# Kernel tuning notes

Measured on AMD Instinct MI355X. Metric: run time of the kernel, lower is better.

Reference implementation:

```python
import jax, jax.numpy as jnp
import numpy as np

B, T_IN, T_OUT, V, C = 2048, 10, 25, 22, 3
D = V * C            # embed / gru hidden = 66
H = 3                # attention heads
HD = D // H          # head dim = 22
EPS = 1e-5
DIMS = [(C, 64), (64, 32), (32, 64), (64, C)]


def _bn(x, g, b):
    # eval-mode BatchNorm2d with default running stats (mean=0, var=1)
    return x * (g / jnp.sqrt(1.0 + EPS))[None, :, None, None] + b[None, :, None, None]


def _gcn_layer(x, A, Tm, cw, cb, g, bt, rw, rb, rg, rbt, pre):
    # x: (N, Cin, T, V); STSGCN ST_GCNN_layer with 1x1 conv (kernel [1,1])
    res = _bn(jnp.einsum('nctv,oc->notv', x, rw) + rb[None, :, None, None], rg, rbt)
    y = jnp.einsum('nctv,vtq->ncqv', x, Tm)   # temporal mixing
    y = jnp.einsum('nctv,tvw->nctw', y, A)    # spatial (joint) mixing
    y = _bn(jnp.einsum('nctv,oc->notv', y, cw) + cb[None, :, None, None], g, bt)
    y = y + res
    return jnp.where(y >= 0, y, pre * y)      # PReLU (scalar slope)


def setup_inputs() -> dict:
    key = jax.random.key(0)
    ks = iter(jax.random.split(key, 64))
    def rn(shape, s=0.05):
        return jax.random.normal(next(ks), shape, dtype=jnp.float32) * s
    d = {"x": rn((B, T_IN, V, C), 1.0)}
    d["A"] = rn((4, T_IN, V, V), 0.2)
    d["Tm"] = rn((4, V, T_IN, T_IN), 0.3)
    d["pre"] = jnp.full((4,), 0.25, jnp.float32)
    for i, (ci, co) in enumerate(DIMS):
        d[f"cw{i}"] = rn((co, ci), 0.1)
        d[f"cb{i}"] = rn((co,), 0.1)
        d[f"g{i}"] = jnp.ones((co,), jnp.float32)
        d[f"bt{i}"] = jnp.zeros((co,), jnp.float32)
        d[f"rw{i}"] = rn((co, ci), 0.1)
        d[f"rb{i}"] = rn((co,), 0.1)
        d[f"rg{i}"] = jnp.ones((co,), jnp.float32)
        d[f"rbt{i}"] = jnp.zeros((co,), jnp.float32)
    d["gru_wi"] = rn((3 * D, D)); d["gru_wh"] = rn((3 * D, D))
    d["gru_bi"] = rn((3 * D,));   d["gru_bh"] = rn((3 * D,))
    d["qkv_w"] = rn((3 * D, D)); d["qkv_b"] = rn((3 * D,))
    d["ow"] = rn((D, D)); d["ob"] = rn((D,))
    d["lw"] = rn((D, 2 * D)); d["lb"] = rn((D,))
    return d


def _forward(x, A, Tm, pre, cws, cbs, gs, bts, rws, rbs, rgs, rbts,
             gru_wi, gru_wh, gru_bi, gru_bh, qkv_w, qkv_b, ow, ob, lw, lb):
    raw = x.reshape(B, T_IN, D)                 # (N,T,V*C), joint-major flatten
    h = jnp.transpose(x, (0, 3, 1, 2))          # (N,C,T,V)
    for i in range(4):
        h = _gcn_layer(h, A[i], Tm[i], cws[i], cbs[i], gs[i], bts[i],
                       rws[i], rbs[i], rgs[i], rbts[i], pre[i])
    enc = jnp.transpose(h, (0, 2, 3, 1)).reshape(B, T_IN, D)  # (N,T,V*C)

    wq, wk, wv = qkv_w[:D], qkv_w[D:2 * D], qkv_w[2 * D:]
    bq, bk, bv = qkv_b[:D], qkv_b[D:2 * D], qkv_b[2 * D:]
    # K,V of encoder sequence are constant across decode steps: project once
    k = (enc @ wk.T + bk).reshape(B, T_IN, H, HD)
    v = (enc @ wv.T + bv).reshape(B, T_IN, H, HD)
    scale = 1.0 / jnp.sqrt(jnp.float32(HD))

    def gru(inp, hprev):
        gi = inp @ gru_wi.T + gru_bi
        gh = hprev @ gru_wh.T + gru_bh
        ir, iz, inn = jnp.split(gi, 3, axis=-1)
        hr, hz, hn = jnp.split(gh, 3, axis=-1)
        r = jax.nn.sigmoid(ir + hr)
        z = jax.nn.sigmoid(iz + hz)
        n = jnp.tanh(inn + r * hn)
        return (1.0 - z) * n + z * hprev

    def step(carry, _):
        hs, tp = carry
        hs = gru(tp, hs)
        q = ((hs @ wq.T + bq) * scale).reshape(B, H, HD)
        scores = jnp.einsum('bhd,bthd->bht', q, k)
        attn = jax.nn.softmax(scores, axis=-1)
        ctx = jnp.einsum('bht,bthd->bhd', attn, v).reshape(B, D) @ ow.T + ob
        pred = jnp.concatenate([hs, ctx], axis=-1) @ lw.T + lb + tp  # residual
        return (hs, pred), pred

    h0 = enc[:, -1, :]
    tp0 = raw[:, -1, :]
    _, preds = jax.lax.scan(step, (h0, tp0), None, length=T_OUT)
    out = jnp.transpose(preds, (1, 0, 2))       # (N, T_out, D)
    return out.reshape(B, T_OUT, V, C)


def reference(x, A, Tm, pre,
              cw0, cb0, g0, bt0, rw0, rb0, rg0, rbt0,
              cw1, cb1, g1, bt1, rw1, rb1, rg1, rbt1,
              cw2, cb2, g2, bt2, rw2, rb2, rg2, rbt2,
              cw3, cb3, g3, bt3, rw3, rb3, rg3, rbt3,
              gru_wi, gru_wh, gru_bi, gru_bh, qkv_w, qkv_b, ow, ob, lw, lb):
    return _forward(x, A, Tm, pre,
                    [cw0, cw1, cw2, cw3], [cb0, cb1, cb2, cb3],
                    [g0, g1, g2, g3], [bt0, bt1, bt2, bt3],
                    [rw0, rw1, rw2, rw3], [rb0, rb1, rb2, rb3],
                    [rg0, rg1, rg2, rg3], [rbt0, rbt1, rbt2, rbt3],
                    gru_wi, gru_wh, gru_bi, gru_bh, qkv_w, qkv_b, ow, ob, lw, lb)
```

## Files before the change

kernel.cpp:

```cpp
#include <hip/hip_runtime.h>

#define DEV static __device__ __forceinline__


struct EncW {
  const float* cw[4]; const float* cb[4]; const float* g[4]; const float* bt[4];
  const float* rw[4]; const float* rb[4]; const float* rg[4]; const float* rbt[4];
};

template<int CI, int CO, int OGRAN>
DEV void gcn_layer32(int tid,
    const float* __restrict__ cw, const float* __restrict__ cb,
    const float* __restrict__ gg, const float* __restrict__ bt,
    const float* __restrict__ rw, const float* __restrict__ rb,
    const float* __restrict__ rg, const float* __restrict__ rbt,
    const float* __restrict__ TmL, const float* __restrict__ AL, float preL,
    float* __restrict__ act, float* __restrict__ S,
    float* __restrict__ rmul, float* __restrict__ radd,
    float* __restrict__ cmul, float* __restrict__ cadd)
{
  constexpr int COP8 = (CO + 7) & ~7;
  constexpr int NT = (CO / OGRAN) * 55;
  const float inv = 0.99999499987f;

  for (int idx = tid; idx < CI * COP8; idx += 512) {
    int c = idx / COP8, o = idx % COP8;
    S[idx] = (o < CO) ? rw[o * CI + c] : 0.f;
  }
  for (int idx = tid; idx < 64; idx += 512) {
    bool ok = idx < CO;
    float rm = ok ? rg[idx] * inv : 0.f;
    float cm = ok ? gg[idx] * inv : 0.f;
    rmul[idx] = rm;
    radd[idx] = ok ? rb[idx] * rm + rbt[idx] : 0.f;
    cmul[idx] = cm;
    cadd[idx] = ok ? cb[idx] * cm + bt[idx] : 0.f;
  }
  __syncthreads();

  float racc[OGRAN * 4];
  int og = tid / 55, pp = tid % 55;
  if (tid < NT) {
    #pragma unroll
    for (int k = 0; k < OGRAN * 4; ++k) racc[k] = 0.f;
    #pragma unroll 4
    for (int c = 0; c < CI; ++c) {
      const float* wr = S + c * COP8 + og * OGRAN;
      float4 av = *(const float4*)(act + c * 220 + pp * 4);
      float wv[OGRAN];
      if constexpr (OGRAN == 8) {
        float4 w0 = *(const float4*)(wr);
        float4 w1 = *(const float4*)(wr + 4);
        wv[0]=w0.x; wv[1]=w0.y; wv[2]=w0.z; wv[3]=w0.w;
        wv[4]=w1.x; wv[5]=w1.y; wv[6]=w1.z; wv[7]=w1.w;
      } else if constexpr (OGRAN == 4) {
        float4 w0 = *(const float4*)(wr);
        wv[0]=w0.x; wv[1]=w0.y; wv[2]=w0.z; wv[3]=w0.w;
      } else {
        wv[0] = wr[0];
      }
      #pragma unroll
      for (int o = 0; o < OGRAN; ++o) {
        racc[o*4+0] += wv[o]*av.x; racc[o*4+1] += wv[o]*av.y;
        racc[o*4+2] += wv[o]*av.z; racc[o*4+3] += wv[o]*av.w;
      }
    }
    #pragma unroll
    for (int o = 0; o < OGRAN; ++o) {
      float m = rmul[og * OGRAN + o], a = radd[og * OGRAN + o];
      #pragma unroll
      for (int k = 0; k < 4; ++k) racc[o*4+k] = racc[o*4+k]*m + a;
    }
  }
  __syncthreads();

  for (int idx = tid; idx < 2200; idx += 512) {
    int tq = idx / 22, v = idx % 22;
    int t = tq / 10, q = tq % 10;
    S[idx] = TmL[v * 100 + t * 10 + q];
  }
  __syncthreads();

  for (int idx = tid; idx < CI * 11; idx += 512) {
    int v2 = idx % 11, c = idx / 11;
    float* base = act + c * 220 + v2 * 2;
    float xin[10][2];
    #pragma unroll
    for (int t = 0; t < 10; ++t) { xin[t][0] = base[t*22]; xin[t][1] = base[t*22+1]; }
    float ya[10][2];
    #pragma unroll
    for (int q = 0; q < 10; ++q) { ya[q][0] = 0.f; ya[q][1] = 0.f; }
    #pragma unroll
    for (int t = 0; t < 10; ++t) {
      const float* tm = S + t * 220 + v2 * 2;
      #pragma unroll
      for (int q = 0; q < 10; ++q) {
        ya[q][0] += tm[q*22]   * xin[t][0];
        ya[q][1] += tm[q*22+1] * xin[t][1];
      }
    }
    #pragma unroll
    for (int q = 0; q < 10; ++q) { base[q*22] = ya[q][0]; base[q*22+1] = ya[q][1]; }
  }
  __syncthreads();

  for (int idx = tid; idx < 4840; idx += 512) S[idx] = AL[idx];
  __syncthreads();

  for (int idx = tid; idx < CI * 10; idx += 512) {
    int t = idx % 10, c = idx / 10;
    float* row = act + c * 220 + t * 22;
    float yin[22];
    #pragma unroll
    for (int v = 0; v < 22; ++v) yin[v] = row[v];
    float za[22];
    #pragma unroll
    for (int w = 0; w < 22; ++w) za[w] = 0.f;
    #pragma unroll 2
    for (int v = 0; v < 22; ++v) {
      const float* ar = S + (t * 22 + v) * 22;
      float y0 = yin[v];
      #pragma unroll
      for (int w = 0; w < 22; ++w) za[w] += y0 * ar[w];
    }
    #pragma unroll
    for (int w = 0; w < 22; ++w) row[w] = za[w];
  }
  __syncthreads();

  for (int idx = tid; idx < CI * COP8; idx += 512) {
    int c = idx / COP8, o = idx % COP8;
    S[idx] = (o < CO) ? cw[o * CI + c] : 0.f;
  }
  __syncthreads();

  float cacc[OGRAN * 4];
  if (tid < NT) {
    #pragma unroll
    for (int k = 0; k < OGRAN * 4; ++k) cacc[k] = 0.f;
    #pragma unroll 4
    for (int c = 0; c < CI; ++c) {
      const float* wr = S + c * COP8 + og * OGRAN;
      float4 av = *(const float4*)(act + c * 220 + pp * 4);
      float wv[OGRAN];
      if constexpr (OGRAN == 8) {
        float4 w0 = *(const float4*)(wr);
        float4 w1 = *(const float4*)(wr + 4);
        wv[0]=w0.x; wv[1]=w0.y; wv[2]=w0.z; wv[3]=w0.w;
        wv[4]=w1.x; wv[5]=w1.y; wv[6]=w1.z; wv[7]=w1.w;
      } else if constexpr (OGRAN == 4) {
        float4 w0 = *(const float4*)(wr);
        wv[0]=w0.x; wv[1]=w0.y; wv[2]=w0.z; wv[3]=w0.w;
      } else {
        wv[0] = wr[0];
      }
      #pragma unroll
      for (int o = 0; o < OGRAN; ++o) {
        cacc[o*4+0] += wv[o]*av.x; cacc[o*4+1] += wv[o]*av.y;
        cacc[o*4+2] += wv[o]*av.z; cacc[o*4+3] += wv[o]*av.w;
      }
    }
  }
  __syncthreads();
  if (tid < NT) {
    #pragma unroll
    for (int o = 0; o < OGRAN; ++o) {
      float m = cmul[og * OGRAN + o], a = cadd[og * OGRAN + o];
      #pragma unroll
      for (int k = 0; k < 4; ++k) {
        float y = cacc[o*4+k]*m + a + racc[o*4+k];
        act[(og*OGRAN+o)*220 + pp*4 + k] = (y >= 0.f) ? y : preL * y;
      }
    }
  }
  __syncthreads();
}

__global__ __launch_bounds__(512, 4)
void enc_kernel(const float* __restrict__ x, const float* __restrict__ A,
                const float* __restrict__ Tm, const float* __restrict__ pre, EncW W,
                const float* __restrict__ qkvT, const float* __restrict__ qkv_b,
                float* __restrict__ h0_ws, float* __restrict__ k_ws,
                float* __restrict__ v_ws)
{
  __shared__ __align__(16) float act[64 * 220];
  __shared__ __align__(16) float S[4840];
  __shared__ float rmul[64], radd[64], cmul[64], cadd[64];

  const int tid = threadIdx.x;
  const int b = blockIdx.x;

  for (int idx = tid; idx < 660; idx += 512) {
    int c = idx / 220, r = idx % 220, t = r / 22, v = r % 22;
    act[c * 220 + t * 22 + v] = x[(((size_t)b * 10 + t) * 22 + v) * 3 + c];
  }
  float p0 = pre[0], p1 = pre[1], p2 = pre[2], p3 = pre[3];

  gcn_layer32<3, 64, 8>(tid, W.cw[0], W.cb[0], W.g[0], W.bt[0], W.rw[0], W.rb[0], W.rg[0], W.rbt[0],
                        Tm, A, p0, act, S, rmul, radd, cmul, cadd);
  gcn_layer32<64, 32, 4>(tid, W.cw[1], W.cb[1], W.g[1], W.bt[1], W.rw[1], W.rb[1], W.rg[1], W.rbt[1],
                        Tm + 2200, A + 4840, p1, act, S, rmul, radd, cmul, cadd);
  gcn_layer32<32, 64, 8>(tid, W.cw[2], W.cb[2], W.g[2], W.bt[2], W.rw[2], W.rb[2], W.rg[2], W.rbt[2],
                        Tm + 4400, A + 9680, p2, act, S, rmul, radd, cmul, cadd);
  gcn_layer32<64, 3, 1>(tid, W.cw[3], W.cb[3], W.g[3], W.bt[3], W.rw[3], W.rb[3], W.rg[3], W.rbt[3],
                        Tm + 6600, A + 14520, p3, act, S, rmul, radd, cmul, cadd);

  float* encD = act + 3 * 220;
  for (int idx = tid; idx < 660; idx += 512) {
    int t = idx / 66, d = idx % 66, v = d / 3, c = d % 3;
    float val = act[c * 220 + t * 22 + v];
    encD[idx] = val;
    if (t == 9) h0_ws[(size_t)b * 66 + d] = val;
  }
  __syncthreads();

  for (int idx = tid; idx < 1320; idx += 512) {
    const int t = idx / 132, dd = idx % 132;
    const int row = 66 + dd;
    const float* wp = qkvT + row;
    const float* ep = encD + t * 66;
    float acc = 0.f;
    #pragma unroll 6
    for (int e = 0; e < 66; ++e) acc += wp[e * 198] * ep[e];
    acc += qkv_b[row];
    const int half = dd / 66, d = dd - half * 66;
    float* dst = half ? v_ws : k_ws;
    dst[(size_t)b * 660 + t * 66 + d] = acc;
  }
}


__global__ __launch_bounds__(512)
void prep_kernel(const float* __restrict__ qkv_w, const float* __restrict__ ow,
                 const float* __restrict__ ob, const float* __restrict__ lw,
                 const float* __restrict__ gru_wi, const float* __restrict__ gru_wh,
                 float* __restrict__ qkvT, float* __restrict__ wqD,
                 float* __restrict__ lwAT, float* __restrict__ MT,
                 float* __restrict__ cb2, float* __restrict__ wT_g)
{
  int idx = blockIdx.x * 512 + threadIdx.x;
  if (idx < 13068) {
    int e = idx / 198, j = idx % 198;
    qkvT[idx] = qkv_w[j * 66 + e];
    return;
  }
  int i1 = idx - 13068;
  if (i1 < 4356) {
    int e = i1 / 66, d = i1 % 66;
    wqD[i1] = qkv_w[d * 66 + e];
    return;
  }
  int i2 = i1 - 4356;
  if (i2 < 4356) {
    int e = i2 / 66, d = i2 % 66;
    lwAT[i2] = lw[d * 132 + e];
    return;
  }
  int i3 = i2 - 4356;
  if (i3 < 4356) {
    int e = i3 / 66, d = i3 % 66;
    const float* lrow = lw + d * 132 + 66;
    float acc = 0.f;
    for (int f = 0; f < 66; ++f) acc += lrow[f] * ow[f * 66 + e];
    MT[i3] = acc;
    return;
  }
  int i4 = i3 - 4356;
  if (i4 < 66) {
    const float* lrow = lw + i4 * 132 + 66;
    float acc = 0.f;
    for (int f = 0; f < 66; ++f) acc += lrow[f] * ob[f];
    cb2[i4] = acc;
    return;
  }
  int i5 = i4 - 66;
  if (i5 < 26136) {
    int e = i5 / 396, jm = i5 % 396;
    wT_g[i5] = (jm < 198) ? gru_wi[jm * 66 + e] : gru_wh[(jm - 198) * 66 + e];
  }
}


__global__ __launch_bounds__(512, 4)
void dec_kernel(const float* __restrict__ x, const float* __restrict__ h0_ws,
                const float* __restrict__ k_ws, const float* __restrict__ v_ws,
                const float* __restrict__ wT_g,
                const float* __restrict__ gru_bi, const float* __restrict__ gru_bh,
                const float* __restrict__ wqD, const float* __restrict__ qkv_b,
                const float* __restrict__ lwAT, const float* __restrict__ MT,
                const float* __restrict__ cb2, const float* __restrict__ lb,
                float* __restrict__ outp)
{
  __shared__ __align__(16) float wqS[4356];
  __shared__ __align__(16) float lwAS[4356];
  __shared__ __align__(16) float MS[4356];
  __shared__ __align__(16) float kS[2640];
  __shared__ __align__(16) float G[396 * 4];
  __shared__ __align__(16) float tpT[264], hsT[264], qT[264], cxT[264];
  __shared__ float attnS[120];
  __shared__ float biS[198], bhS[198], bqS[66], lbS[66];

  const int tid = threadIdx.x;
  const int b0 = blockIdx.x * 4;

  for (int idx = tid; idx < 4356; idx += 512) {
    wqS[idx] = wqD[idx]; lwAS[idx] = lwAT[idx]; MS[idx] = MT[idx];
  }
  for (int idx = tid; idx < 2640; idx += 512) {
    int r = idx / 660, rest = idx % 660;
    kS[idx] = k_ws[(size_t)(b0 + r) * 660 + rest];
  }
  for (int idx = tid; idx < 198; idx += 512) { biS[idx] = gru_bi[idx]; bhS[idx] = gru_bh[idx]; }
  for (int idx = tid; idx < 66; idx += 512)  { bqS[idx] = qkv_b[idx]; lbS[idx] = lb[idx] + cb2[idx]; }
  for (int idx = tid; idx < 264; idx += 512) {
    int d = idx >> 2, r = idx & 3;
    hsT[d * 4 + r] = h0_ws[(size_t)(b0 + r) * 66 + d];
    tpT[d * 4 + r] = x[(size_t)(b0 + r) * 660 + 594 + d];
  }
  __syncthreads();

  const float qscale = 1.0f / sqrtf(22.0f);

  for (int s = 0; s < 25; ++s) {
    if (tid < 396) {
      const float* base = (tid < 198) ? tpT : hsT;
      const float* wp = wT_g + tid;
      float a0 = 0.f, a1 = 0.f, a2 = 0.f, a3 = 0.f;
      #pragma unroll 11
      for (int e = 0; e < 66; ++e) {
        float w = wp[e * 396];
        float4 av = *(const float4*)(base + e * 4);
        a0 += w * av.x; a1 += w * av.y; a2 += w * av.z; a3 += w * av.w;
      }
      float bias = (tid < 198) ? biS[tid] : bhS[tid - 198];
      *(float4*)(G + tid * 4) = make_float4(a0 + bias, a1 + bias, a2 + bias, a3 + bias);
    }
    __syncthreads();

    if (tid < 264) {
      int d = tid >> 2, r = tid & 3;
      float ir = G[d * 4 + r]         + G[(198 + d) * 4 + r];
      float iz = G[(66 + d) * 4 + r]  + G[(264 + d) * 4 + r];
      float nx = G[(132 + d) * 4 + r];
      float hn = G[(330 + d) * 4 + r];
      float rg = 1.f / (1.f + __expf(-ir));
      float zg = 1.f / (1.f + __expf(-iz));
      float t2 = __expf(2.f * (nx + rg * hn));
      float ng = 1.f - 2.f / (t2 + 1.f);
      float h = hsT[d * 4 + r];
      hsT[d * 4 + r] = (1.f - zg) * ng + zg * h;
    }
    __syncthreads();

    if (tid < 264) {
      int r = tid / 66, d = tid % 66;
      float acc = 0.f;
      #pragma unroll 6
      for (int e = 0; e < 66; ++e)
        acc += wqS[e * 66 + d] * hsT[e * 4 + r];
      qT[d * 4 + r] = (acc + bqS[d]) * qscale;
    }
    __syncthreads();

    if (tid < 120) {
      int r = tid / 30, rem = tid % 30, h = rem / 10, t = rem % 10;
      const float* kp = kS + r * 660 + t * 66 + h * 22;
      const float* qp = qT + (h * 22) * 4 + r;
      float acc = 0.f;
      #pragma unroll
      for (int dd = 0; dd < 22; ++dd) acc += qp[dd * 4] * kp[dd];
      attnS[(r * 3 + h) * 10 + t] = acc;
    }
    __syncthreads();

    if (tid < 12) {
      float* sp = attnS + tid * 10;
      float mx = sp[0];
      #pragma unroll
      for (int t = 1; t < 10; ++t) mx = fmaxf(mx, sp[t]);
      float sum = 0.f;
      #pragma unroll
      for (int t = 0; t < 10; ++t) { float e = __expf(sp[t] - mx); sp[t] = e; sum += e; }
      float invs = 1.f / sum;
      #pragma unroll
      for (int t = 0; t < 10; ++t) sp[t] *= invs;
    }
    __syncthreads();

    if (tid < 264) {
      int r = tid / 66, d = tid % 66, h = d / 22;
      const float* ap = attnS + (r * 3 + h) * 10;
      const float* vp = v_ws + (size_t)(b0 + r) * 660 + d;
      float acc = 0.f;
      #pragma unroll
      for (int t = 0; t < 10; ++t) acc += ap[t] * vp[t * 66];
      cxT[d * 4 + r] = acc;
    }
    __syncthreads();

    if (tid < 264) {
      int r = tid / 66, d = tid % 66;
      float acc = 0.f;
      #pragma unroll 6
      for (int e = 0; e < 66; ++e)
        acc += lwAS[e * 66 + d] * hsT[e * 4 + r] + MS[e * 66 + d] * cxT[e * 4 + r];
      float pred = acc + lbS[d] + tpT[d * 4 + r];
      outp[((size_t)(b0 + r) * 25 + s) * 66 + d] = pred;
      tpT[d * 4 + r] = pred;
    }
    __syncthreads();
  }
}


extern "C" void kernel_launch(void* const* d_in, const int* in_sizes, int n_in,
                              void* d_out, int out_size, void* d_ws, size_t ws_size,
                              hipStream_t stream) {
  (void)in_sizes; (void)n_in; (void)out_size; (void)ws_size;
  const float* x   = (const float*)d_in[0];
  const float* A   = (const float*)d_in[1];
  const float* Tm  = (const float*)d_in[2];
  const float* pre = (const float*)d_in[3];
  EncW W;
  for (int i = 0; i < 4; ++i) {
    W.cw[i]  = (const float*)d_in[4 + 8 * i + 0];
    W.cb[i]  = (const float*)d_in[4 + 8 * i + 1];
    W.g[i]   = (const float*)d_in[4 + 8 * i + 2];
    W.bt[i]  = (const float*)d_in[4 + 8 * i + 3];
    W.rw[i]  = (const float*)d_in[4 + 8 * i + 4];
    W.rb[i]  = (const float*)d_in[4 + 8 * i + 5];
    W.rg[i]  = (const float*)d_in[4 + 8 * i + 6];
    W.rbt[i] = (const float*)d_in[4 + 8 * i + 7];
  }
  const float* gru_wi = (const float*)d_in[36];
  const float* gru_wh = (const float*)d_in[37];
  const float* gru_bi = (const float*)d_in[38];
  const float* gru_bh = (const float*)d_in[39];
  const float* qkv_w  = (const float*)d_in[40];
  const float* qkv_b  = (const float*)d_in[41];
  const float* ow     = (const float*)d_in[42];
  const float* ob     = (const float*)d_in[43];
  const float* lw     = (const float*)d_in[44];
  const float* lb     = (const float*)d_in[45];

  float* wsf  = (float*)d_ws;
  float* h0   = wsf;
  float* kw   = h0 + 2048 * 66;
  float* vw   = kw + 2048 * 660;
  float* qkvT = vw + 2048 * 660;
  float* wqD  = qkvT + 13068;
  float* lwAT = wqD + 4356;
  float* MT   = lwAT + 4356;
  float* cb2  = MT + 4356;
  float* wT_g = cb2 + 66;

  prep_kernel<<<103, 512, 0, stream>>>(qkv_w, ow, ob, lw, gru_wi, gru_wh,
                                       qkvT, wqD, lwAT, MT, cb2, wT_g);
  enc_kernel<<<2048, 512, 0, stream>>>(x, A, Tm, pre, W, qkvT, qkv_b, h0, kw, vw);
  dec_kernel<<<512, 512, 0, stream>>>(x, h0, kw, vw, wT_g, gru_bi, gru_bh,
                                      wqD, qkv_b, lwAT, MT, cb2, lb,
                                      (float*)d_out);
}
```

Measured before the change: 703.3 us.

## Halve decoder rows per block, co-stage Tm with residual weights, cheaper thread mapping

The decoder now handles 2 batch rows per block instead of 4 and launches 1024 blocks with a higher occupancy hint. Its shared memory shrinks because lwA and M are read straight from global memory. This is meant to spread the serial 25-step recurrence across more CUs and raise occupancy, at the cost of more repeated weight loading and global reads per step. In the encoder, the temporal-mixing matrix is staged together with the residual weights, which removes one sync and load phase per layer. The og/pp thread mapping also switches to bit ops where there are 8 groups.

```diff
diff --git a/kernel.cpp b/kernel.cpp
--- a/kernel.cpp
+++ b/kernel.cpp
@@ -8,7 +8,7 @@
   const float* rw[4]; const float* rb[4]; const float* rg[4]; const float* rbt[4];
 };
 
-template<int CI, int CO, int OGRAN>
+template<int CI, int CO, int OGRAN, bool OGFAST>
 DEV void gcn_layer32(int tid,
     const float* __restrict__ cw, const float* __restrict__ cb,
     const float* __restrict__ gg, const float* __restrict__ bt,
@@ -20,12 +20,22 @@
     float* __restrict__ cmul, float* __restrict__ cadd)
 {
   constexpr int COP8 = (CO + 7) & ~7;
-  constexpr int NT = (CO / OGRAN) * 55;
+  constexpr int NG = CO / OGRAN;
+  constexpr int NT = NG * 55;
+  constexpr int RWN = CI * COP8;
+  static_assert(!OGFAST || NG == 8, "OGFAST requires NG==8");
+  static_assert(RWN + 2200 <= 4840, "rw+Tm co-stage must fit in S");
   const float inv = 0.99999499987f;
 
-  for (int idx = tid; idx < CI * COP8; idx += 512) {
-    int c = idx / COP8, o = idx % COP8;
-    S[idx] = (o < CO) ? rw[o * CI + c] : 0.f;
+  for (int idx = tid; idx < RWN + 2200; idx += 512) {
+    if (idx < RWN) {
+      int c = idx / COP8, o = idx % COP8;
+      S[idx] = (o < CO) ? rw[o * CI + c] : 0.f;
+    } else {
+      int j = idx - RWN;
+      int tq = j / 22, v = j % 22;
+      S[idx] = TmL[v * 100 + tq];
+    }
   }
   for (int idx = tid; idx < 64; idx += 512) {
     bool ok = idx < CO;
@@ -39,7 +49,8 @@
   __syncthreads();
 
   float racc[OGRAN * 4];
-  int og = tid / 55, pp = tid % 55;
+  const int og = OGFAST ? (tid & 7) : (tid / 55);
+  const int pp = OGFAST ? (tid >> 3) : (tid % 55);
   if (tid < NT) {
     #pragma unroll
     for (int k = 0; k < OGRAN * 4; ++k) racc[k] = 0.f;
@@ -74,13 +85,6 @@
   }
   __syncthreads();
 
-  for (int idx = tid; idx < 2200; idx += 512) {
-    int tq = idx / 22, v = idx % 22;
-    int t = tq / 10, q = tq % 10;
-    S[idx] = TmL[v * 100 + t * 10 + q];
-  }
-  __syncthreads();
-
   for (int idx = tid; idx < CI * 11; idx += 512) {
     int v2 = idx % 11, c = idx / 11;
     float* base = act + c * 220 + v2 * 2;
@@ -92,7 +96,7 @@
     for (int q = 0; q < 10; ++q) { ya[q][0] = 0.f; ya[q][1] = 0.f; }
     #pragma unroll
     for (int t = 0; t < 10; ++t) {
-      const float* tm = S + t * 220 + v2 * 2;
+      const float* tm = S + RWN + t * 220 + v2 * 2;
       #pragma unroll
       for (int q = 0; q < 10; ++q) {
         ya[q][0] += tm[q*22]   * xin[t][0];
@@ -128,7 +132,7 @@
   }
   __syncthreads();
 
-  for (int idx = tid; idx < CI * COP8; idx += 512) {
+  for (int idx = tid; idx < RWN; idx += 512) {
     int c = idx / COP8, o = idx % COP8;
     S[idx] = (o < CO) ? cw[o * CI + c] : 0.f;
   }
@@ -196,13 +200,13 @@
   }
   float p0 = pre[0], p1 = pre[1], p2 = pre[2], p3 = pre[3];
 
-  gcn_layer32<3, 64, 8>(tid, W.cw[0], W.cb[0], W.g[0], W.bt[0], W.rw[0], W.rb[0], W.rg[0], W.rbt[0],
+  gcn_layer32<3, 64, 8, true>(tid, W.cw[0], W.cb[0], W.g[0], W.bt[0], W.rw[0], W.rb[0], W.rg[0], W.rbt[0],
                         Tm, A, p0, act, S, rmul, radd, cmul, cadd);
-  gcn_layer32<64, 32, 4>(tid, W.cw[1], W.cb[1], W.g[1], W.bt[1], W.rw[1], W.rb[1], W.rg[1], W.rbt[1],
+  gcn_layer32<64, 32, 4, true>(tid, W.cw[1], W.cb[1], W.g[1], W.bt[1], W.rw[1], W.rb[1], W.rg[1], W.rbt[1],
                         Tm + 2200, A + 4840, p1, act, S, rmul, radd, cmul, cadd);
-  gcn_layer32<32, 64, 8>(tid, W.cw[2], W.cb[2], W.g[2], W.bt[2], W.rw[2], W.rb[2], W.rg[2], W.rbt[2],
+  gcn_layer32<32, 64, 8, true>(tid, W.cw[2], W.cb[2], W.g[2], W.bt[2], W.rw[2], W.rb[2], W.rg[2], W.rbt[2],
                         Tm + 4400, A + 9680, p2, act, S, rmul, radd, cmul, cadd);
-  gcn_layer32<64, 3, 1>(tid, W.cw[3], W.cb[3], W.g[3], W.bt[3], W.rw[3], W.rb[3], W.rg[3], W.rbt[3],
+  gcn_layer32<64, 3, 1, false>(tid, W.cw[3], W.cb[3], W.g[3], W.bt[3], W.rw[3], W.rb[3], W.rg[3], W.rbt[3],
                         Tm + 6600, A + 14520, p3, act, S, rmul, radd, cmul, cadd);
 
   float* encD = act + 3 * 220;
@@ -281,7 +285,7 @@
 }
 
 
-__global__ __launch_bounds__(512, 4)
+__global__ __launch_bounds__(512, 8)
 void dec_kernel(const float* __restrict__ x, const float* __restrict__ h0_ws,
                 const float* __restrict__ k_ws, const float* __restrict__ v_ws,
                 const float* __restrict__ wT_g,
@@ -292,30 +296,26 @@
                 float* __restrict__ outp)
 {
   __shared__ __align__(16) float wqS[4356];
-  __shared__ __align__(16) float lwAS[4356];
-  __shared__ __align__(16) float MS[4356];
-  __shared__ __align__(16) float kS[2640];
-  __shared__ __align__(16) float G[396 * 4];
-  __shared__ __align__(16) float tpT[264], hsT[264], qT[264], cxT[264];
-  __shared__ float attnS[120];
+  __shared__ __align__(16) float kS[1320];
+  __shared__ __align__(16) float G[396 * 2];
+  __shared__ __align__(16) float tpT[132], hsT[132], qT[132], cxT[132];
+  __shared__ float attnS[60];
   __shared__ float biS[198], bhS[198], bqS[66], lbS[66];
 
   const int tid = threadIdx.x;
-  const int b0 = blockIdx.x * 4;
-
-  for (int idx = tid; idx < 4356; idx += 512) {
-    wqS[idx] = wqD[idx]; lwAS[idx] = lwAT[idx]; MS[idx] = MT[idx];
-  }
-  for (int idx = tid; idx < 2640; idx += 512) {
+  const int b0 = blockIdx.x * 2;
+
+  for (int idx = tid; idx < 4356; idx += 512) wqS[idx] = wqD[idx];
+  for (int idx = tid; idx < 1320; idx += 512) {
     int r = idx / 660, rest = idx % 660;
     kS[idx] = k_ws[(size_t)(b0 + r) * 660 + rest];
   }
   for (int idx = tid; idx < 198; idx += 512) { biS[idx] = gru_bi[idx]; bhS[idx] = gru_bh[idx]; }
   for (int idx = tid; idx < 66; idx += 512)  { bqS[idx] = qkv_b[idx]; lbS[idx] = lb[idx] + cb2[idx]; }
-  for (int idx = tid; idx < 264; idx += 512) {
-    int d = idx >> 2, r = idx & 3;
-    hsT[d * 4 + r] = h0_ws[(size_t)(b0 + r) * 66 + d];
-    tpT[d * 4 + r] = x[(size_t)(b0 + r) * 660 + 594 + d];
+  for (int idx = tid; idx < 132; idx += 512) {
+    int d = idx >> 1, r = idx & 1;
+    hsT[d * 2 + r] = h0_ws[(size_t)(b0 + r) * 66 + d];
+    tpT[d * 2 + r] = x[(size_t)(b0 + r) * 660 + 594 + d];
   }
   __syncthreads();
 
@@ -325,55 +325,55 @@
     if (tid < 396) {
       const float* base = (tid < 198) ? tpT : hsT;
       const float* wp = wT_g + tid;
-      float a0 = 0.f, a1 = 0.f, a2 = 0.f, a3 = 0.f;
+      float a0 = 0.f, a1 = 0.f;
       #pragma unroll 11
       for (int e = 0; e < 66; ++e) {
         float w = wp[e * 396];
-        float4 av = *(const float4*)(base + e * 4);
-        a0 += w * av.x; a1 += w * av.y; a2 += w * av.z; a3 += w * av.w;
+        float2 av = *(const float2*)(base + e * 2);
+        a0 += w * av.x; a1 += w * av.y;
       }
       float bias = (tid < 198) ? biS[tid] : bhS[tid - 198];
-      *(float4*)(G + tid * 4) = make_float4(a0 + bias, a1 + bias, a2 + bias, a3 + bias);
-    }
-    __syncthreads();
-
-    if (tid < 264) {
-      int d = tid >> 2, r = tid & 3;
-      float ir = G[d * 4 + r]         + G[(198 + d) * 4 + r];
-      float iz = G[(66 + d) * 4 + r]  + G[(264 + d) * 4 + r];
-      float nx = G[(132 + d) * 4 + r];
-      float hn = G[(330 + d) * 4 + r];
+      *(float2*)(G + tid * 2) = make_float2(a0 + bias, a1 + bias);
+    }
+    __syncthreads();
+
+    if (tid < 132) {
+      int d = tid >> 1, r = tid & 1;
+      float ir = G[d * 2 + r]         + G[(198 + d) * 2 + r];
+      float iz = G[(66 + d) * 2 + r]  + G[(264 + d) * 2 + r];
+      float nx = G[(132 + d) * 2 + r];
+      float hn = G[(330 + d) * 2 + r];
       float rg = 1.f / (1.f + __expf(-ir));
       float zg = 1.f / (1.f + __expf(-iz));
       float t2 = __expf(2.f * (nx + rg * hn));
       float ng = 1.f - 2.f / (t2 + 1.f);
-      float h = hsT[d * 4 + r];
-      hsT[d * 4 + r] = (1.f - zg) * ng + zg * h;
-    }
-    __syncthreads();
-
-    if (tid < 264) {
+      float h = hsT[d * 2 + r];
+      hsT[d * 2 + r] = (1.f - zg) * ng + zg * h;
+    }
+    __syncthreads();
+
+    if (tid < 132) {
       int r = tid / 66, d = tid % 66;
       float acc = 0.f;
       #pragma unroll 6
       for (int e = 0; e < 66; ++e)
-        acc += wqS[e * 66 + d] * hsT[e * 4 + r];
-      qT[d * 4 + r] = (acc + bqS[d]) * qscale;
-    }
-    __syncthreads();
-
-    if (tid < 120) {
+        acc += wqS[e * 66 + d] * hsT[e * 2 + r];
+      qT[d * 2 + r] = (acc + bqS[d]) * qscale;
+    }
+    __syncthreads();
+
+    if (tid < 60) {
       int r = tid / 30, rem = tid % 30, h = rem / 10, t = rem % 10;
       const float* kp = kS + r * 660 + t * 66 + h * 22;
-      const float* qp = qT + (h * 22) * 4 + r;
+      const float* qp = qT + (h * 22) * 2 + r;
       float acc = 0.f;
       #pragma unroll
-      for (int dd = 0; dd < 22; ++dd) acc += qp[dd * 4] * kp[dd];
+      for (int dd = 0; dd < 22; ++dd) acc += qp[dd * 2] * kp[dd];
       attnS[(r * 3 + h) * 10 + t] = acc;
     }
     __syncthreads();
 
-    if (tid < 12) {
+    if (tid < 6) {
       float* sp = attnS + tid * 10;
       float mx = sp[0];
       #pragma unroll
@@ -387,26 +387,26 @@
     }
     __syncthreads();
 
-    if (tid < 264) {
+    if (tid < 132) {
       int r = tid / 66, d = tid % 66, h = d / 22;
       const float* ap = attnS + (r * 3 + h) * 10;
       const float* vp = v_ws + (size_t)(b0 + r) * 660 + d;
       float acc = 0.f;
       #pragma unroll
       for (int t = 0; t < 10; ++t) acc += ap[t] * vp[t * 66];
-      cxT[d * 4 + r] = acc;
-    }
-    __syncthreads();
-
-    if (tid < 264) {
+      cxT[d * 2 + r] = acc;
+    }
+    __syncthreads();
+
+    if (tid < 132) {
       int r = tid / 66, d = tid % 66;
       float acc = 0.f;
       #pragma unroll 6
       for (int e = 0; e < 66; ++e)
-        acc += lwAS[e * 66 + d] * hsT[e * 4 + r] + MS[e * 66 + d] * cxT[e * 4 + r];
-      float pred = acc + lbS[d] + tpT[d * 4 + r];
+        acc += lwAT[e * 66 + d] * hsT[e * 2 + r] + MT[e * 66 + d] * cxT[e * 2 + r];
+      float pred = acc + lbS[d] + tpT[d * 2 + r];
       outp[((size_t)(b0 + r) * 25 + s) * 66 + d] = pred;
-      tpT[d * 4 + r] = pred;
+      tpT[d * 2 + r] = pred;
     }
     __syncthreads();
   }
@@ -457,7 +457,7 @@
   prep_kernel<<<103, 512, 0, stream>>>(qkv_w, ow, ob, lw, gru_wi, gru_wh,
                                        qkvT, wqD, lwAT, MT, cb2, wT_g);
   enc_kernel<<<2048, 512, 0, stream>>>(x, A, Tm, pre, W, qkvT, qkv_b, h0, kw, vw);
-  dec_kernel<<<512, 512, 0, stream>>>(x, h0, kw, vw, wT_g, gru_bi, gru_bh,
-                                      wqD, qkv_b, lwAT, MT, cb2, lb,
-                                      (float*)d_out);
+  dec_kernel<<<1024, 512, 0, stream>>>(x, h0, kw, vw, wT_g, gru_bi, gru_bh,
+                                       wqD, qkv_b, lwAT, MT, cb2, lb,
+                                       (float*)d_out);
 }
```

Measured after the change: 905.2 us. +28.7%, slower.

## Reorder channel-reducing GCN layers to mix after projecting, co-stage Tm with weights

Applied to the files above, without the earlier changes.

For layers where output channels are fewer than input channels (64->32, 64->3), the 1x1 conv and residual projections are computed first as one fused GEMM. The temporal and joint mixing then run on CO channels instead of CI, which is valid because the mixing is linear and commutes with the channel projection. For the other layers, the Tm staging is merged into the residual-weight staging loop to remove one barrier. The cost is an extra elementwise combine pass, and the reordered layers keep 2*CO channels live in shared memory.

```diff
diff --git a/kernel.cpp b/kernel.cpp
--- a/kernel.cpp
+++ b/kernel.cpp
@@ -8,8 +8,9 @@
   const float* rw[4]; const float* rb[4]; const float* rg[4]; const float* rbt[4];
 };
 
+
 template<int CI, int CO, int OGRAN>
-DEV void gcn_layer32(int tid,
+DEV void gcn_orig(int tid,
     const float* __restrict__ cw, const float* __restrict__ cb,
     const float* __restrict__ gg, const float* __restrict__ bt,
     const float* __restrict__ rw, const float* __restrict__ rb,
@@ -21,11 +22,19 @@
 {
   constexpr int COP8 = (CO + 7) & ~7;
   constexpr int NT = (CO / OGRAN) * 55;
+  constexpr int RWN = CI * COP8;
+  static_assert(RWN + 2200 <= 4840, "rw+Tm co-stage must fit in S");
   const float inv = 0.99999499987f;
 
-  for (int idx = tid; idx < CI * COP8; idx += 512) {
-    int c = idx / COP8, o = idx % COP8;
-    S[idx] = (o < CO) ? rw[o * CI + c] : 0.f;
+  for (int idx = tid; idx < RWN + 2200; idx += 512) {
+    if (idx < RWN) {
+      int c = idx / COP8, o = idx % COP8;
+      S[idx] = (o < CO) ? rw[o * CI + c] : 0.f;
+    } else {
+      int j = idx - RWN;
+      int tq = j / 22, v = j % 22;
+      S[idx] = TmL[v * 100 + tq];
+    }
   }
   for (int idx = tid; idx < 64; idx += 512) {
     bool ok = idx < CO;
@@ -39,7 +48,7 @@
   __syncthreads();
 
   float racc[OGRAN * 4];
-  int og = tid / 55, pp = tid % 55;
+  const int og = tid / 55, pp = tid % 55;
   if (tid < NT) {
     #pragma unroll
     for (int k = 0; k < OGRAN * 4; ++k) racc[k] = 0.f;
@@ -74,13 +83,6 @@
   }
   __syncthreads();
 
-  for (int idx = tid; idx < 2200; idx += 512) {
-    int tq = idx / 22, v = idx % 22;
-    int t = tq / 10, q = tq % 10;
-    S[idx] = TmL[v * 100 + t * 10 + q];
-  }
-  __syncthreads();
-
   for (int idx = tid; idx < CI * 11; idx += 512) {
     int v2 = idx % 11, c = idx / 11;
     float* base = act + c * 220 + v2 * 2;
@@ -92,7 +94,7 @@
     for (int q = 0; q < 10; ++q) { ya[q][0] = 0.f; ya[q][1] = 0.f; }
     #pragma unroll
     for (int t = 0; t < 10; ++t) {
-      const float* tm = S + t * 220 + v2 * 2;
+      const float* tm = S + RWN + t * 220 + v2 * 2;
       #pragma unroll
       for (int q = 0; q < 10; ++q) {
         ya[q][0] += tm[q*22]   * xin[t][0];
@@ -128,7 +130,7 @@
   }
   __syncthreads();
 
-  for (int idx = tid; idx < CI * COP8; idx += 512) {
+  for (int idx = tid; idx < RWN; idx += 512) {
     int c = idx / COP8, o = idx % COP8;
     S[idx] = (o < CO) ? cw[o * CI + c] : 0.f;
   }
@@ -176,6 +178,145 @@
   __syncthreads();
 }
 
+template<int CI, int CO, int OGRAN>
+DEV void gcn_reord(int tid,
+    const float* __restrict__ cw, const float* __restrict__ cb,
+    const float* __restrict__ gg, const float* __restrict__ bt,
+    const float* __restrict__ rw, const float* __restrict__ rb,
+    const float* __restrict__ rg, const float* __restrict__ rbt,
+    const float* __restrict__ TmL, const float* __restrict__ AL, float preL,
+    float* __restrict__ act, float* __restrict__ S,
+    float* __restrict__ rmul, float* __restrict__ radd,
+    float* __restrict__ cmul, float* __restrict__ cadd)
+{
+  constexpr int CO2 = 2 * CO;
+  constexpr int COP8 = (CO2 + 7) & ~7;
+  constexpr int NT = (CO2 / OGRAN) * 55;
+  constexpr int RWN = CI * COP8;
+  static_assert(RWN <= 4840, "W2 must fit in S");
+  const float inv = 0.99999499987f;
+
+  for (int idx = tid; idx < RWN; idx += 512) {
+    int c = idx / COP8, o = idx % COP8;
+    float w = 0.f;
+    if (o < CO) w = cw[o * CI + c];
+    else if (o < CO2) w = rw[(o - CO) * CI + c];
+    S[idx] = w;
+  }
+  for (int idx = tid; idx < 64; idx += 512) {
+    bool ok = idx < CO;
+    float rm = ok ? rg[idx] * inv : 0.f;
+    float cm = ok ? gg[idx] * inv : 0.f;
+    rmul[idx] = rm;
+    radd[idx] = ok ? rb[idx] * rm + rbt[idx] : 0.f;
+    cmul[idx] = cm;
+    cadd[idx] = ok ? cb[idx] * cm + bt[idx] : 0.f;
+  }
+  __syncthreads();
+
+  float acc[OGRAN * 4];
+  const int og = tid / 55, pp = tid % 55;
+  if (tid < NT) {
+    #pragma unroll
+    for (int k = 0; k < OGRAN * 4; ++k) acc[k] = 0.f;
+    #pragma unroll 4
+    for (int c = 0; c < CI; ++c) {
+      const float* wr = S + c * COP8 + og * OGRAN;
+      float4 av = *(const float4*)(act + c * 220 + pp * 4);
+      float wv[OGRAN];
+      if constexpr (OGRAN == 8) {
+        float4 w0 = *(const float4*)(wr);
+        float4 w1 = *(const float4*)(wr + 4);
+        wv[0]=w0.x; wv[1]=w0.y; wv[2]=w0.z; wv[3]=w0.w;
+        wv[4]=w1.x; wv[5]=w1.y; wv[6]=w1.z; wv[7]=w1.w;
+      } else if constexpr (OGRAN == 4) {
+        float4 w0 = *(const float4*)(wr);
+        wv[0]=w0.x; wv[1]=w0.y; wv[2]=w0.z; wv[3]=w0.w;
+      } else {
+        wv[0] = wr[0];
+      }
+      #pragma unroll
+      for (int o = 0; o < OGRAN; ++o) {
+        acc[o*4+0] += wv[o]*av.x; acc[o*4+1] += wv[o]*av.y;
+        acc[o*4+2] += wv[o]*av.z; acc[o*4+3] += wv[o]*av.w;
+      }
+    }
+  }
+  __syncthreads();
+
+  if (tid < NT) {
+    #pragma unroll
+    for (int o = 0; o < OGRAN; ++o) {
+      const int oo = og * OGRAN + o;
+      const bool isr = oo >= CO;
+      const float m = isr ? rmul[oo - CO] : 1.f;
+      const float a = isr ? radd[oo - CO] : 0.f;
+      #pragma unroll
+      for (int k = 0; k < 4; ++k)
+        act[oo * 220 + pp * 4 + k] = acc[o*4+k] * m + a;
+    }
+  }
+  for (int i = tid; i < 2200; i += 512) {
+    int tq = i / 22, v = i % 22;
+    S[i] = TmL[v * 100 + tq];
+  }
+  __syncthreads();
+
+  for (int idx = tid; idx < CO * 11; idx += 512) {
+    int v2 = idx % 11, c = idx / 11;
+    float* base = act + c * 220 + v2 * 2;
+    float xin[10][2];
+    #pragma unroll
+    for (int t = 0; t < 10; ++t) { xin[t][0] = base[t*22]; xin[t][1] = base[t*22+1]; }
+    float ya[10][2];
+    #pragma unroll
+    for (int q = 0; q < 10; ++q) { ya[q][0] = 0.f; ya[q][1] = 0.f; }
+    #pragma unroll
+    for (int t = 0; t < 10; ++t) {
+      const float* tm = S + t * 220 + v2 * 2;
+      #pragma unroll
+      for (int q = 0; q < 10; ++q) {
+        ya[q][0] += tm[q*22]   * xin[t][0];
+        ya[q][1] += tm[q*22+1] * xin[t][1];
+      }
+    }
+    #pragma unroll
+    for (int q = 0; q < 10; ++q) { base[q*22] = ya[q][0]; base[q*22+1] = ya[q][1]; }
+  }
+  __syncthreads();
+
+  for (int idx = tid; idx < 4840; idx += 512) S[idx] = AL[idx];
+  __syncthreads();
+
+  for (int idx = tid; idx < CO * 10; idx += 512) {
+    int t = idx % 10, c = idx / 10;
+    float* row = act + c * 220 + t * 22;
+    float yin[22];
+    #pragma unroll
+    for (int v = 0; v < 22; ++v) yin[v] = row[v];
+    float za[22];
+    #pragma unroll
+    for (int w = 0; w < 22; ++w) za[w] = 0.f;
+    #pragma unroll 2
+    for (int v = 0; v < 22; ++v) {
+      const float* ar = S + (t * 22 + v) * 22;
+      float y0 = yin[v];
+      #pragma unroll
+      for (int w = 0; w < 22; ++w) za[w] += y0 * ar[w];
+    }
+    #pragma unroll
+    for (int w = 0; w < 22; ++w) row[w] = za[w];
+  }
+  __syncthreads();
+
+  for (int idx = tid; idx < CO * 220; idx += 512) {
+    int o = idx / 220, p = idx % 220;
+    float y = act[o * 220 + p] * cmul[o] + cadd[o] + act[(CO + o) * 220 + p];
+    act[o * 220 + p] = (y >= 0.f) ? y : preL * y;
+  }
+  __syncthreads();
+}
+
 __global__ __launch_bounds__(512, 4)
 void enc_kernel(const float* __restrict__ x, const float* __restrict__ A,
                 const float* __restrict__ Tm, const float* __restrict__ pre, EncW W,
@@ -196,14 +337,14 @@
   }
   float p0 = pre[0], p1 = pre[1], p2 = pre[2], p3 = pre[3];
 
-  gcn_layer32<3, 64, 8>(tid, W.cw[0], W.cb[0], W.g[0], W.bt[0], W.rw[0], W.rb[0], W.rg[0], W.rbt[0],
-                        Tm, A, p0, act, S, rmul, radd, cmul, cadd);
-  gcn_layer32<64, 32, 4>(tid, W.cw[1], W.cb[1], W.g[1], W.bt[1], W.rw[1], W.rb[1], W.rg[1], W.rbt[1],
-                        Tm + 2200, A + 4840, p1, act, S, rmul, radd, cmul, cadd);
-  gcn_layer32<32, 64, 8>(tid, W.cw[2], W.cb[2], W.g[2], W.bt[2], W.rw[2], W.rb[2], W.rg[2], W.rbt[2],
-                        Tm + 4400, A + 9680, p2, act, S, rmul, radd, cmul, cadd);
-  gcn_layer32<64, 3, 1>(tid, W.cw[3], W.cb[3], W.g[3], W.bt[3], W.rw[3], W.rb[3], W.rg[3], W.rbt[3],
-                        Tm + 6600, A + 14520, p3, act, S, rmul, radd, cmul, cadd);
+  gcn_orig<3, 64, 8>(tid, W.cw[0], W.cb[0], W.g[0], W.bt[0], W.rw[0], W.rb[0], W.rg[0], W.rbt[0],
+                     Tm, A, p0, act, S, rmul, radd, cmul, cadd);
+  gcn_reord<64, 32, 8>(tid, W.cw[1], W.cb[1], W.g[1], W.bt[1], W.rw[1], W.rb[1], W.rg[1], W.rbt[1],
+                     Tm + 2200, A + 4840, p1, act, S, rmul, radd, cmul, cadd);
+  gcn_orig<32, 64, 8>(tid, W.cw[2], W.cb[2], W.g[2], W.bt[2], W.rw[2], W.rb[2], W.rg[2], W.rbt[2],
+                     Tm + 4400, A + 9680, p2, act, S, rmul, radd, cmul, cadd);
+  gcn_reord<64, 3, 1>(tid, W.cw[3], W.cb[3], W.g[3], W.bt[3], W.rw[3], W.rb[3], W.rg[3], W.rbt[3],
+                     Tm + 6600, A + 14520, p3, act, S, rmul, radd, cmul, cadd);
 
   float* encD = act + 3 * 220;
   for (int idx = tid; idx < 660; idx += 512) {
```

Result: faster. 657.8 us (-6.5%).
